# Optimization experiments

Measured on AMD Instinct MI355X. Metric: run time of the kernel, lower is better.

## Reference

```python
import jax, jax.numpy as jnp
import numpy as np

BIG_DIST = 1.0e7      # replaces NaN entries of the distance matrix (torch: where(isnan, 1e7))
BIG_DIFF = 10000.0    # nan_to_num value for cyclic coordinate error
MATCH_SAMPLE_NUM = 128


def setup_inputs() -> dict:
    key = jax.random.key(0)
    k1, k2, k3, k4, k5, k6 = jax.random.split(key, 6)
    b, h, w, c = 8, 64, 64, 384
    hw = h * w
    K = MATCH_SAMPLE_NUM
    return {
        "feature1": jax.random.normal(k1, (b, h, w, c), dtype=jnp.float32),
        "feature2": jax.random.normal(k2, (b, h, w, c), dtype=jnp.float32),
        "mask1": jax.random.randint(k3, (b, h, w, 1), 0, 2).astype(jnp.int32),
        "mask2": jax.random.randint(k4, (b, h, w, 1), 0, 2).astype(jnp.int32),
        "choose_backup1": jax.random.randint(k5, (b, K), 0, hw).astype(jnp.int32),
        "choose_backup2": jax.random.randint(k6, (b, K), 0, hw).astype(jnp.int32),
    }


def _masked_cdist(feature1, feature2, m1, m2):
    """Euclidean cdist of L2-normalized features; pairs touching a masked-out
    token get BIG_DIST (equivalent to torch's NaN-fill -> isnan -> 1e7)."""
    b, h, w, c = feature1.shape
    hw = h * w
    f1 = feature1.reshape(b, hw, c)
    f2 = feature2.reshape(b, hw, c)
    f1 = f1 / jnp.linalg.norm(f1, axis=-1, keepdims=True)
    f2 = f2 / jnp.linalg.norm(f2, axis=-1, keepdims=True)
    f1 = jnp.where(m1[..., None], f1, 0.0)
    f2 = jnp.where(m2[..., None], f2, 0.0)
    sq1 = jnp.sum(f1 * f1, axis=-1)              # [b, hw]
    sq2 = jnp.sum(f2 * f2, axis=-1)              # [b, hw]
    dots = jnp.einsum("bic,bjc->bij", f1, f2)    # [b, hw, hw]
    d2 = sq1[:, :, None] + sq2[:, None, :] - 2.0 * dots
    d = jnp.sqrt(jnp.maximum(d2, 0.0))
    valid_pair = m1[:, :, None] & m2[:, None, :]
    return jnp.where(valid_pair, d, BIG_DIST)


def _cyclic_diff(match_fwd, match_bwd, m_src, m_dst, h, w):
    """Cyclic-consistency coordinate error for each source token."""
    b, hw = match_fwd.shape
    # cyclic index: src -> dst (match_fwd) -> back to src (match_bwd gathered)
    dst_valid = jnp.take_along_axis(m_dst, match_fwd, axis=1)           # [b, hw]
    cyc = jnp.take_along_axis(match_bwd, match_fwd, axis=1)             # [b, hw]
    cx = (cyc // w).astype(jnp.float32)
    cy = (cyc % w).astype(jnp.float32)
    idx = jnp.arange(hw)
    gx = (idx // w).astype(jnp.float32)[None, :]
    gy = (idx % w).astype(jnp.float32)[None, :]
    diff = jnp.sqrt((cx - gx) ** 2 + (cy - gy) ** 2)
    valid = m_src & dst_valid
    return jnp.where(valid, diff, BIG_DIFF)


def reference(feature1, feature2, mask1, mask2, choose_backup1, choose_backup2):
    b, h, w, c = feature1.shape
    hw = h * w
    K = MATCH_SAMPLE_NUM
    m1 = mask1.reshape(b, hw) > 0
    m2 = mask2.reshape(b, hw) > 0

    d = _masked_cdist(feature1, feature2, m1, m2)   # [b, hw, hw]
    match1 = jnp.argmin(d, axis=-1)                 # best j for each i, [b, hw]
    match2 = jnp.argmin(d, axis=-2)                 # best i for each j, [b, hw]

    coord_diff1 = _cyclic_diff(match1, match2, m1, m2, h, w)
    coord_diff2 = _cyclic_diff(match2, match1, m2, m1, h, w)

    choose1 = jax.lax.top_k(-coord_diff1, K)[1]
    choose1 = jnp.where((jnp.sum(m1, axis=-1) >= K)[:, None], choose1, choose_backup1)
    choose1_match = jnp.take_along_axis(match1, choose1, axis=1)

    choose2 = jax.lax.top_k(-coord_diff2, K)[1]
    choose2 = jnp.where((jnp.sum(m2, axis=-1) >= K)[:, None], choose2, choose_backup2)
    choose2_match = jnp.take_along_axis(match2, choose2, axis=1)

    out_match1 = jnp.stack([choose1, choose1_match], axis=-1)   # [b, K, 2]
    out_match2 = jnp.stack([choose2, choose2_match], axis=-1)   # [b, K, 2]
    return out_match1, out_match2
```

## Files before the change

kernel.cpp:

```cpp
#include <hip/hip_runtime.h>
#include <stdint.h>

#define HW 4096
#define CH 384
#define NB 8
#define K_SEL 128
#define BIG_DIST 1.0e7f
#define BIG_DIFF 10000.0f
#define PAGE 8192
#define NKB 12
#define NRB 32

typedef unsigned long long u64;
typedef _Float16 f16;
typedef _Float16 f16x8 __attribute__((ext_vector_type(8)));
typedef float f32x4 __attribute__((ext_vector_type(4)));

__device__ __forceinline__ u64 encode_di(float d, int idx) {
    return ((u64)__float_as_uint(d) << 32) | (unsigned)idx;
}

__device__ __forceinline__ void gl_lds16(const void* g, void* l) {
    __builtin_amdgcn_global_load_lds(
        (const __attribute__((address_space(1))) unsigned int*)g,
        (__attribute__((address_space(3))) unsigned int*)l, 16, 0, 0);
}

__device__ __forceinline__ int swz(int row, int bytecol) {
    return (row * 64 + bytecol) ^ ((row & 7) << 4);
}

__global__ __launch_bounds__(1024)
void compact_mask(const int* __restrict__ mask1, const int* __restrict__ mask2,
                  int* __restrict__ vidx1, int* __restrict__ vidx2,
                  int* __restrict__ cpos1, int* __restrict__ cpos2,
                  u64* __restrict__ slot1, u64* __restrict__ slot2,
                  int* __restrict__ cnts) {
    const int b = blockIdx.x, which = blockIdx.y;
    const int* m = (which ? mask2 : mask1) + (size_t)b * HW;
    int* vidx = (which ? vidx2 : vidx1) + (size_t)b * HW;
    int* cpos = (which ? cpos2 : cpos1) + (size_t)b * HW;
    u64* slot = (which ? slot2 : slot1) + (size_t)b * HW;
    const int tid = threadIdx.x;
    const int lane = tid & 63, wv = tid >> 6;

    const int base = tid * 4;
    int4 mm = *(const int4*)(m + base);
    int v0 = mm.x > 0, v1 = mm.y > 0, v2 = mm.z > 0, v3 = mm.w > 0;
    int sum = v0 + v1 + v2 + v3;

    int inc = sum;
#pragma unroll
    for (int off = 1; off < 64; off <<= 1) {
        int o = __shfl_up(inc, off, 64);
        if (lane >= off) inc += o;
    }
    __shared__ int wtot[16], wbase[16];
    if (lane == 63) wtot[wv] = inc;
    __syncthreads();
    if (tid == 0) {
        int acc = 0;
        for (int w = 0; w < 16; ++w) { wbase[w] = acc; acc += wtot[w]; }
        cnts[b * 2 + which] = acc;
    }
    __syncthreads();
    int pos = wbase[wv] + inc - sum;
    if (v0) { vidx[pos] = base;     cpos[base]     = pos; pos++; } else cpos[base]     = -1;
    if (v1) { vidx[pos] = base + 1; cpos[base + 1] = pos; pos++; } else cpos[base + 1] = -1;
    if (v2) { vidx[pos] = base + 2; cpos[base + 2] = pos; pos++; } else cpos[base + 2] = -1;
    if (v3) { vidx[pos] = base + 3; cpos[base + 3] = pos; pos++; } else cpos[base + 3] = -1;
    __syncthreads();
    const int cnt = wbase[15] + wtot[15];
    for (int t = cnt + tid; t < HW; t += 1024) vidx[t] = 0;
    for (int t = tid; t < HW; t += 1024) slot[t] = ~0ULL;
}

__global__ __launch_bounds__(1024)
void prep_tiles(const float* __restrict__ f1, const float* __restrict__ f2,
                const int* __restrict__ vidx1, const int* __restrict__ vidx2,
                const int* __restrict__ cnts,
                float* __restrict__ sqc1, float* __restrict__ sqc2,
                char* __restrict__ tA, char* __restrict__ tB) {
    const int lin = blockIdx.x;
    const int rb = lin % NRB;
    const int b = lin / NRB;
    const int which = blockIdx.y;
    const int cnt = cnts[b * 2 + which];
    const int rowbase = rb * 128;
    if (rowbase >= cnt) return;

    const float* f = which ? f2 : f1;
    const int* vidx = (which ? vidx2 : vidx1) + (size_t)b * HW;
    float* sqc = which ? sqc2 : sqc1;
    char* pages = (which ? tB : tA) + (size_t)lin * NKB * 2 * PAGE;
    const size_t bb = (size_t)b * HW;

    const int tid = threadIdx.x;
    const int r = tid >> 3;
    const int kq = tid & 7;
    const int gr = rowbase + r;
    const int valid = gr < cnt;
    const int grow = vidx[gr];
    const float* rowp = f + (bb + grow) * CH + kq * 4;

    float4 x4[12];
    float s = 0.f;
#pragma unroll
    for (int kb = 0; kb < NKB; ++kb) {
        float4 v = *(const float4*)(rowp + kb * 32);
        x4[kb] = v;
        s += v.x * v.x + v.y * v.y + v.z * v.z + v.w * v.w;
    }
    s += __shfl_xor(s, 1, 64);
    s += __shfl_xor(s, 2, 64);
    s += __shfl_xor(s, 4, 64);
    float rinv = 1.0f / __fsqrt_rn(s);
    float s2 = 0.f;
#pragma unroll
    for (int kb = 0; kb < NKB; ++kb) {
        float4 v = x4[kb];
        float ax = v.x * rinv, ay = v.y * rinv, az = v.z * rinv, aw = v.w * rinv;
        s2 += ax * ax + ay * ay + az * az + aw * aw;
    }
    s2 += __shfl_xor(s2, 1, 64);
    s2 += __shfl_xor(s2, 2, 64);
    s2 += __shfl_xor(s2, 4, 64);
    if (kq == 0) sqc[bb + gr] = valid ? s2 : 0.f;

    const float rv = valid ? rinv : 0.f;
    const int off = swz(r, kq * 8);
#pragma unroll
    for (int kb = 0; kb < NKB; ++kb) {
        char* hipg = pages + (size_t)kb * 2 * PAGE;
        char* lopg = hipg + PAGE;
        float4 v = x4[kb];
        float ax = v.x * rv, ay = v.y * rv, az = v.z * rv, aw = v.w * rv;
        f16 h0 = (f16)ax, h1 = (f16)ay, h2 = (f16)az, h3 = (f16)aw;
        f16 l0 = (f16)((ax - (float)h0) * 2048.0f);
        f16 l1 = (f16)((ay - (float)h1) * 2048.0f);
        f16 l2 = (f16)((az - (float)h2) * 2048.0f);
        f16 l3 = (f16)((aw - (float)h3) * 2048.0f);
        union { f16 h[4]; uint2 u; } H = {{h0, h1, h2, h3}};
        union { f16 h[4]; uint2 u; } L = {{l0, l1, l2, l3}};
        *(uint2*)(hipg + off) = H.u;
        *(uint2*)(lopg + off) = L.u;
    }
}

__global__ __launch_bounds__(256, 3)
void gemm_argmin(const char* __restrict__ tA, const char* __restrict__ tB,
                 const float* __restrict__ sqc1, const float* __restrict__ sqc2,
                 const int* __restrict__ vidx1, const int* __restrict__ vidx2,
                 const int* __restrict__ cnts,
                 u64* __restrict__ slot1, u64* __restrict__ slot2) {
    __shared__ __align__(16) char smem[4 * PAGE];
    __shared__ u64 rowSlot[128];
    __shared__ u64 colSlot[128];

    const int b = blockIdx.y;
    const int tid = threadIdx.x;

    const int cnt1 = cnts[b * 2], cnt2 = cnts[b * 2 + 1];
    const int nby = (cnt1 + 127) >> 7;
    const int nbx = (cnt2 + 127) >> 7;
    const int nact = nby * nbx;

    const int xcd = blockIdx.x & 7;
    const int s = blockIdx.x >> 3;
    const int q = nact >> 3, r8 = nact & 7;
    const int csz = q + (xcd < r8 ? 1 : 0);
    if (s >= csz) return;
    const int L = (xcd < r8 ? xcd * (q + 1) : r8 * (q + 1) + (xcd - r8) * q) + s;
    const int bx = L / nby;
    const int by = L - bx * nby;
    const int brow = by * 128, bcol = bx * 128;

    if (tid < 128) { rowSlot[tid] = ~0ULL; colSlot[tid] = ~0ULL; }

    const char* Abase = tA + (size_t)(b * NRB + by) * NKB * 2 * PAGE;
    const char* Bbase = tB + (size_t)(b * NRB + bx) * NKB * 2 * PAGE;

    const int wv = tid >> 6, lane = tid & 63;
    const int wr = wv >> 1, wc = wv & 1;
    const int r0 = lane & 15, kc = lane >> 4;

    int aoff[4], boff[4];
#pragma unroll
    for (int m = 0; m < 4; ++m) {
        int ra = wr * 64 + m * 16 + r0;
        aoff[m] = swz(ra, kc * 16);
        int rb_ = wc * 64 + m * 16 + r0;
        boff[m] = swz(rb_, kc * 16);
    }

    f32x4 acc[4][4];
    f32x4 zero = {0.f, 0.f, 0.f, 0.f};
#pragma unroll
    for (int m = 0; m < 4; ++m)
#pragma unroll
        for (int n = 0; n < 4; ++n) acc[m][n] = zero;

    const int stg = wv * 1024;
    const int src_l = stg + lane * 16;
    const f16 K2048 = (f16)2048.0f;

    for (int kb = 0; kb < NKB; ++kb) {
        const char* gA = Abase + (size_t)kb * 2 * PAGE;
        const char* gB = Bbase + (size_t)kb * 2 * PAGE;
#pragma unroll
        for (int p = 0; p < 4; ++p) {
            gl_lds16(gA + p * 4096 + src_l, smem + p * 4096 + stg);
            gl_lds16(gB + p * 4096 + src_l, smem + 16384 + p * 4096 + stg);
        }
        asm volatile("s_waitcnt vmcnt(0)" ::: "memory");
        __syncthreads();

        f16x8 bh[4], bl[4];
#pragma unroll
        for (int n = 0; n < 4; ++n) {
            bh[n] = *(const f16x8*)(smem + 2 * PAGE + boff[n]);
            bl[n] = *(const f16x8*)(smem + 3 * PAGE + boff[n]);
        }
#pragma unroll
        for (int m = 0; m < 4; ++m) {
            f16x8 ah = *(const f16x8*)(smem + aoff[m]);
            f16x8 al = *(const f16x8*)(smem + PAGE + aoff[m]);
            f16x8 ah2 = ah * K2048;
#pragma unroll
            for (int n = 0; n < 4; ++n) {
                acc[m][n] = __builtin_amdgcn_mfma_f32_16x16x32_f16(ah2, bh[n], acc[m][n], 0, 0, 0);
                acc[m][n] = __builtin_amdgcn_mfma_f32_16x16x32_f16(ah, bl[n], acc[m][n], 0, 0, 0);
                acc[m][n] = __builtin_amdgcn_mfma_f32_16x16x32_f16(al, bh[n], acc[m][n], 0, 0, 0);
            }
        }
        __syncthreads();
    }

    const size_t bb = (size_t)b * HW;
    const int rfrag = kc * 4;
    float s1v[4][4];
    int o1v[4][4], val1[4][4];
#pragma unroll
    for (int m = 0; m < 4; ++m) {
        int rr = brow + wr * 64 + m * 16 + rfrag;
        float4 sv = *(const float4*)(sqc1 + bb + rr);
        int4 ov = *(const int4*)(vidx1 + bb + rr);
        s1v[m][0] = sv.x; s1v[m][1] = sv.y; s1v[m][2] = sv.z; s1v[m][3] = sv.w;
        o1v[m][0] = ov.x; o1v[m][1] = ov.y; o1v[m][2] = ov.z; o1v[m][3] = ov.w;
#pragma unroll
        for (int j = 0; j < 4; ++j) val1[m][j] = (rr + j) < cnt1;
    }
    float s2v[4];
    int o2v[4], val2[4];
#pragma unroll
    for (int n = 0; n < 4; ++n) {
        int cc = bcol + wc * 64 + n * 16 + r0;
        s2v[n] = sqc2[bb + cc];
        o2v[n] = vidx2[bb + cc];
        val2[n] = cc < cnt2;
    }

    u64 cbest[4] = {~0ULL, ~0ULL, ~0ULL, ~0ULL};
#pragma unroll
    for (int m = 0; m < 4; ++m) {
#pragma unroll
        for (int j = 0; j < 4; ++j) {
            u64 rbest = ~0ULL;
#pragma unroll
            for (int n = 0; n < 4; ++n) {
                float d;
                if (val1[m][j] && val2[n]) {
                    float dot = acc[m][n][j] * (1.0f / 2048.0f);
                    float t = __fmul_rn(2.0f, dot);
                    float d2 = __fsub_rn(__fadd_rn(s1v[m][j], s2v[n]), t);
                    d = __fsqrt_rn(fmaxf(d2, 0.0f));
                } else {
                    d = BIG_DIST;
                }
                u64 er = encode_di(d, o2v[n]);
                u64 ec = encode_di(d, o1v[m][j]);
                if (er < rbest) rbest = er;
                if (ec < cbest[n]) cbest[n] = ec;
            }
            atomicMin(&rowSlot[wr * 64 + m * 16 + rfrag + j], rbest);
        }
    }
#pragma unroll
    for (int n = 0; n < 4; ++n)
        atomicMin(&colSlot[wc * 64 + n * 16 + r0], cbest[n]);
    __syncthreads();

    if (tid < 128) atomicMin(&slot1[bb + brow + tid], rowSlot[tid]);
    else           atomicMin(&slot2[bb + bcol + tid - 128], colSlot[tid - 128]);
}

__device__ __forceinline__ int get_match(const u64* __restrict__ slot,
                                         const int* __restrict__ cpos,
                                         size_t bb, int t) {
    int p = cpos[bb + t];
    if (p < 0) return 0;
    u64 sv = slot[bb + p];
    return (sv != ~0ULL) ? (int)(unsigned)(sv & 0xFFFFFFFFu) : 0;
}

__global__ __launch_bounds__(1024)
void topk_output(const u64* __restrict__ slot1, const u64* __restrict__ slot2,
                 const int* __restrict__ cpos1, const int* __restrict__ cpos2,
                 const int* __restrict__ mask1, const int* __restrict__ mask2,
                 const int* __restrict__ backup1, const int* __restrict__ backup2,
                 int* __restrict__ out) {
    __shared__ u64 keys[HW];
    __shared__ u64 sel[K_SEL];
    __shared__ int hist[256];
    __shared__ int cnt, selc, sbuck, srank;
    const int b = blockIdx.x;
    const int dir = blockIdx.y;
    const u64* slotF = dir ? slot2 : slot1;
    const u64* slotB = dir ? slot1 : slot2;
    const int* cposF = dir ? cpos2 : cpos1;
    const int* cposB = dir ? cpos1 : cpos2;
    const int* maskS = dir ? mask2 : mask1;
    const int* maskD = dir ? mask1 : mask2;
    const int* backup = dir ? backup2 : backup1;
    const int tid = threadIdx.x;
    const size_t bb = (size_t)b * HW;

    if (tid == 0) { cnt = 0; selc = 0; }
    __syncthreads();
    int local = 0;
    for (int t = tid; t < HW; t += 1024) {
        int mf = get_match(slotF, cposF, bb, t);
        int dv = maskD[bb + mf];
        int cyc = get_match(slotB, cposB, bb, mf);
        float gx = (float)(t >> 6), gy = (float)(t & 63);
        float dx = (float)(cyc >> 6) - gx;
        float dy = (float)(cyc & 63) - gy;
        float diff = __fsqrt_rn(dx * dx + dy * dy);
        int ms = maskS[bb + t];
        float v = (ms > 0 && dv > 0) ? diff : BIG_DIFF;
        keys[t] = ((u64)__float_as_uint(v) << 12) | (unsigned)t;
        local += (ms > 0) ? 1 : 0;
    }
    atomicAdd(&cnt, local);
    __syncthreads();

    u64 prefix = 0;
    int rank = 127;
    for (int shift = 40; shift >= 0; shift -= 8) {
        for (int h = tid; h < 256; h += 1024) hist[h] = 0;
        __syncthreads();
        for (int t = tid; t < HW; t += 1024) {
            u64 k = keys[t];
            bool match = (shift == 40) || ((k >> (shift + 8)) == prefix);
            if (match) atomicAdd(&hist[(int)((k >> shift) & 255)], 1);
        }
        __syncthreads();
        if (tid < 64) {
            int v0 = hist[tid * 4 + 0], v1 = hist[tid * 4 + 1];
            int v2 = hist[tid * 4 + 2], v3 = hist[tid * 4 + 3];
            int s4 = v0 + v1 + v2 + v3;
            int inc = s4;
#pragma unroll
            for (int off = 1; off < 64; off <<= 1) {
                int o = __shfl_up(inc, off, 64);
                if (tid >= off) inc += o;
            }
            int c0 = inc - s4;
            int c1 = c0 + v0, c2 = c1 + v1, c3 = c2 + v2, c4 = c3 + v3;
            if (rank >= c0 && rank < c1)      { sbuck = tid * 4 + 0; srank = rank - c0; }
            else if (rank >= c1 && rank < c2) { sbuck = tid * 4 + 1; srank = rank - c1; }
            else if (rank >= c2 && rank < c3) { sbuck = tid * 4 + 2; srank = rank - c2; }
            else if (rank >= c3 && rank < c4) { sbuck = tid * 4 + 3; srank = rank - c3; }
        }
        __syncthreads();
        prefix = (prefix << 8) | (unsigned)sbuck;
        rank = srank;
        __syncthreads();
    }
    const u64 pivot = prefix;

    for (int t = tid; t < HW; t += 1024) {
        u64 k = keys[t];
        if (k <= pivot) { int p = atomicAdd(&selc, 1); sel[p] = k; }
    }
    __syncthreads();

    for (unsigned kk = 2; kk <= K_SEL; kk <<= 1) {
        for (unsigned j = kk >> 1; j > 0; j >>= 1) {
            if (tid < K_SEL) {
                unsigned ixj = tid ^ j;
                if (ixj > tid) {
                    u64 a = sel[tid], c = sel[ixj];
                    bool up = ((tid & kk) == 0);
                    if ((a > c) == up) { sel[tid] = c; sel[ixj] = a; }
                }
            }
            __syncthreads();
        }
    }

    if (tid < K_SEL) {
        int c;
        if (cnt >= K_SEL) c = (int)(sel[tid] & 0xFFF);
        else c = backup[b * K_SEL + tid];
        int cm = get_match(slotF, cposF, bb, c);
        int* o = out + dir * (NB * K_SEL * 2);
        o[(b * K_SEL + tid) * 2 + 0] = c;
        o[(b * K_SEL + tid) * 2 + 1] = cm;
    }
}

extern "C" void kernel_launch(void* const* d_in, const int* in_sizes, int n_in,
                              void* d_out, int out_size, void* d_ws, size_t ws_size,
                              hipStream_t stream) {
    const float* f1 = (const float*)d_in[0];
    const float* f2 = (const float*)d_in[1];
    const int* mask1 = (const int*)d_in[2];
    const int* mask2 = (const int*)d_in[3];
    const int* backup1 = (const int*)d_in[4];
    const int* backup2 = (const int*)d_in[5];
    int* out = (int*)d_out;

    char* ws = (char*)d_ws;
    char* tA = ws;                    ws += (size_t)NB * NRB * NKB * 2 * PAGE;
    char* tB = ws;                    ws += (size_t)NB * NRB * NKB * 2 * PAGE;
    u64* slot1 = (u64*)ws;            ws += (size_t)NB * HW * 8;
    u64* slot2 = (u64*)ws;            ws += (size_t)NB * HW * 8;
    float* sqc1 = (float*)ws;         ws += (size_t)NB * HW * 4;
    float* sqc2 = (float*)ws;         ws += (size_t)NB * HW * 4;
    int* vidx1 = (int*)ws;            ws += (size_t)NB * HW * 4;
    int* vidx2 = (int*)ws;            ws += (size_t)NB * HW * 4;
    int* cpos1 = (int*)ws;            ws += (size_t)NB * HW * 4;
    int* cpos2 = (int*)ws;            ws += (size_t)NB * HW * 4;
    int* cnts = (int*)ws;             ws += 256;

    compact_mask<<<dim3(NB, 2), 1024, 0, stream>>>(mask1, mask2,
                                                   vidx1, vidx2, cpos1, cpos2,
                                                   slot1, slot2, cnts);
    prep_tiles<<<dim3(NB * NRB, 2), 1024, 0, stream>>>(f1, f2, vidx1, vidx2,
                                                       cnts, sqc1, sqc2, tA, tB);
    gemm_argmin<<<dim3(1024, NB), 256, 0, stream>>>(tA, tB, sqc1, sqc2,
                                                    vidx1, vidx2, cnts,
                                                    slot1, slot2);
    topk_output<<<dim3(NB, 2), 1024, 0, stream>>>(slot1, slot2, cpos1, cpos2,
                                                  mask1, mask2, backup1, backup2,
                                                  out);
}
```

Measured before the change: 155.8 us.

## Replace float radix-select top-k with integer squared-distance histogram select

```diff
diff --git a/kernel.cpp b/kernel.cpp
--- a/kernel.cpp
+++ b/kernel.cpp
@@ -6,7 +6,7 @@
 #define NB 8
 #define K_SEL 128
 #define BIG_DIST 1.0e7f
-#define BIG_DIFF 10000.0f
+#define N_SENT 8100
 #define PAGE 8192
 #define NKB 12
 #define NRB 32
@@ -147,7 +147,7 @@
     }
 }
 
-__global__ __launch_bounds__(256, 3)
+__global__ __launch_bounds__(256, 4)
 void gemm_argmin(const char* __restrict__ tA, const char* __restrict__ tB,
                  const float* __restrict__ sqc1, const float* __restrict__ sqc2,
                  const int* __restrict__ vidx1, const int* __restrict__ vidx2,
@@ -309,10 +309,11 @@
                  const int* __restrict__ mask1, const int* __restrict__ mask2,
                  const int* __restrict__ backup1, const int* __restrict__ backup2,
                  int* __restrict__ out) {
-    __shared__ u64 keys[HW];
-    __shared__ u64 sel[K_SEL];
-    __shared__ int hist[256];
-    __shared__ int cnt, selc, sbuck, srank;
+    __shared__ int nkey[HW];
+    __shared__ int hist[8192];
+    __shared__ int sel[K_SEL];
+    __shared__ int wtot[16], wbase[16];
+    __shared__ int cnt, selc, sn, st;
     const int b = blockIdx.x;
     const int dir = blockIdx.y;
     const u64* slotF = dir ? slot2 : slot1;
@@ -323,65 +324,100 @@
     const int* maskD = dir ? mask1 : mask2;
     const int* backup = dir ? backup2 : backup1;
     const int tid = threadIdx.x;
+    const int lane = tid & 63, wv = tid >> 6;
     const size_t bb = (size_t)b * HW;
 
     if (tid == 0) { cnt = 0; selc = 0; }
-    __syncthreads();
+    for (int h = tid; h < 8192; h += 1024) hist[h] = 0;
+    __syncthreads();
+
     int local = 0;
     for (int t = tid; t < HW; t += 1024) {
         int mf = get_match(slotF, cposF, bb, t);
         int dv = maskD[bb + mf];
         int cyc = get_match(slotB, cposB, bb, mf);
-        float gx = (float)(t >> 6), gy = (float)(t & 63);
-        float dx = (float)(cyc >> 6) - gx;
-        float dy = (float)(cyc & 63) - gy;
-        float diff = __fsqrt_rn(dx * dx + dy * dy);
+        int dx = (cyc >> 6) - (t >> 6);
+        int dy = (cyc & 63) - (t & 63);
         int ms = maskS[bb + t];
-        float v = (ms > 0 && dv > 0) ? diff : BIG_DIFF;
-        keys[t] = ((u64)__float_as_uint(v) << 12) | (unsigned)t;
+        int n = (ms > 0 && dv > 0) ? (dx * dx + dy * dy) : N_SENT;
+        nkey[t] = (n << 12) | t;
         local += (ms > 0) ? 1 : 0;
+        atomicAdd(&hist[n], 1);
     }
     atomicAdd(&cnt, local);
     __syncthreads();
 
-    u64 prefix = 0;
     int rank = 127;
-    for (int shift = 40; shift >= 0; shift -= 8) {
-        for (int h = tid; h < 256; h += 1024) hist[h] = 0;
-        __syncthreads();
-        for (int t = tid; t < HW; t += 1024) {
-            u64 k = keys[t];
-            bool match = (shift == 40) || ((k >> (shift + 8)) == prefix);
-            if (match) atomicAdd(&hist[(int)((k >> shift) & 255)], 1);
-        }
-        __syncthreads();
-        if (tid < 64) {
-            int v0 = hist[tid * 4 + 0], v1 = hist[tid * 4 + 1];
-            int v2 = hist[tid * 4 + 2], v3 = hist[tid * 4 + 3];
-            int s4 = v0 + v1 + v2 + v3;
-            int inc = s4;
-#pragma unroll
-            for (int off = 1; off < 64; off <<= 1) {
-                int o = __shfl_up(inc, off, 64);
-                if (tid >= off) inc += o;
+    {
+        const int hbase = tid * 8;
+        int ssum = 0;
+#pragma unroll
+        for (int i = 0; i < 8; ++i) ssum += hist[hbase + i];
+        int inc = ssum;
+#pragma unroll
+        for (int off = 1; off < 64; off <<= 1) {
+            int o = __shfl_up(inc, off, 64);
+            if (lane >= off) inc += o;
+        }
+        if (lane == 63) wtot[wv] = inc;
+        __syncthreads();
+        if (tid == 0) {
+            int acc = 0;
+            for (int w = 0; w < 16; ++w) { wbase[w] = acc; acc += wtot[w]; }
+        }
+        __syncthreads();
+        int pre = wbase[wv] + inc - ssum;
+        if (rank >= pre && rank < pre + ssum) {
+            int rr = rank - pre;
+            for (int i = 0; i < 8; ++i) {
+                int h = hist[hbase + i];
+                if (rr < h) { sn = hbase + i; st = rr; break; }
+                rr -= h;
             }
-            int c0 = inc - s4;
-            int c1 = c0 + v0, c2 = c1 + v1, c3 = c2 + v2, c4 = c3 + v3;
-            if (rank >= c0 && rank < c1)      { sbuck = tid * 4 + 0; srank = rank - c0; }
-            else if (rank >= c1 && rank < c2) { sbuck = tid * 4 + 1; srank = rank - c1; }
-            else if (rank >= c2 && rank < c3) { sbuck = tid * 4 + 2; srank = rank - c2; }
-            else if (rank >= c3 && rank < c4) { sbuck = tid * 4 + 3; srank = rank - c3; }
-        }
-        __syncthreads();
-        prefix = (prefix << 8) | (unsigned)sbuck;
-        rank = srank;
-        __syncthreads();
-    }
-    const u64 pivot = prefix;
+        }
+        __syncthreads();
+    }
+    const int npiv = sn;
+    rank = st;
+    __syncthreads();
+
+    for (int h = tid; h < 4096; h += 1024) hist[h] = 0;
+    __syncthreads();
+    for (int t = tid; t < HW; t += 1024)
+        if ((nkey[t] >> 12) == npiv) hist[t] = 1;
+    __syncthreads();
+    {
+        const int hbase = tid * 4;
+        int ssum = hist[hbase] + hist[hbase + 1] + hist[hbase + 2] + hist[hbase + 3];
+        int inc = ssum;
+#pragma unroll
+        for (int off = 1; off < 64; off <<= 1) {
+            int o = __shfl_up(inc, off, 64);
+            if (lane >= off) inc += o;
+        }
+        if (lane == 63) wtot[wv] = inc;
+        __syncthreads();
+        if (tid == 0) {
+            int acc = 0;
+            for (int w = 0; w < 16; ++w) { wbase[w] = acc; acc += wtot[w]; }
+        }
+        __syncthreads();
+        int pre = wbase[wv] + inc - ssum;
+        if (rank >= pre && rank < pre + ssum) {
+            int rr = rank - pre;
+            for (int i = 0; i < 4; ++i) {
+                int h = hist[hbase + i];
+                if (rr < h) { st = hbase + i; break; }
+                rr -= h;
+            }
+        }
+        __syncthreads();
+    }
+    const int pivot = (npiv << 12) | st;
 
     for (int t = tid; t < HW; t += 1024) {
-        u64 k = keys[t];
-        if (k <= pivot) { int p = atomicAdd(&selc, 1); sel[p] = k; }
+        int k = nkey[t];
+        if (k <= pivot) { int p = atomicAdd(&selc, 1); if (p < K_SEL) sel[p] = k; }
     }
     __syncthreads();
 
@@ -390,7 +426,7 @@
             if (tid < K_SEL) {
                 unsigned ixj = tid ^ j;
                 if (ixj > tid) {
-                    u64 a = sel[tid], c = sel[ixj];
+                    int a = sel[tid], c = sel[ixj];
                     bool up = ((tid & kk) == 0);
                     if ((a > c) == up) { sel[tid] = c; sel[ixj] = a; }
                 }
@@ -401,7 +437,7 @@
 
     if (tid < K_SEL) {
         int c;
-        if (cnt >= K_SEL) c = (int)(sel[tid] & 0xFFF);
+        if (cnt >= K_SEL) c = sel[tid] & 0xFFF;
         else c = backup[b * K_SEL + tid];
         int cm = get_match(slotF, cposF, bb, c);
         int* o = out + dir * (NB * K_SEL * 2);
```

Result: slower. 192.2 us (+23.4%).
